# Kernel tuning notes

Measured on AMD Instinct MI355X. Metric: run time of the kernel, lower is better.

Reference implementation:

```python
import jax, jax.numpy as jnp
import numpy as np

B = 16        # batch
N = 1024      # satellite nodes
D = 256       # hidden size
H = 8         # attention heads
NUM_LAYERS = 3          # config.n_layer_aa
L = NUM_LAYERS + 1      # distinct GAT layers
EPS = 1e-5


def setup_inputs() -> dict:
    key = jax.random.key(0)
    ks = jax.random.split(key, 6)
    graph_vectors = jax.random.normal(ks[0], (B, N + 1, D), dtype=jnp.float32)
    graph = jax.random.uniform(ks[1], (B, N, N), dtype=jnp.float32)
    scale = 0.02
    Wq = jax.random.normal(ks[2], (L, D, D), dtype=jnp.float32) * scale
    Wk = jax.random.normal(ks[3], (L, D, D), dtype=jnp.float32) * scale
    Wv = jax.random.normal(ks[4], (L, D, D), dtype=jnp.float32) * scale
    Wo = jax.random.normal(ks[5], (L, D, D), dtype=jnp.float32) * scale
    ln_g = jnp.ones((L, D), dtype=jnp.float32)
    ln_b = jnp.zeros((L, D), dtype=jnp.float32)
    return {"graph_vectors": graph_vectors, "graph": graph,
            "Wq": Wq, "Wk": Wk, "Wv": Wv, "Wo": Wo,
            "ln_g": ln_g, "ln_b": ln_b}


def _layer_norm(x, g, b):
    mu = jnp.mean(x, axis=-1, keepdims=True)
    var = jnp.var(x, axis=-1, keepdims=True)
    return (x - mu) * jax.lax.rsqrt(var + EPS) * g + b


def _gat(x_q, x_kv, wq, wk, wv, wo, g, b):
    # multi-head attention: x_q [B,Lq,D] attends over x_kv [B,Lk,D]
    Bq, Lq, _ = x_q.shape
    Lk = x_kv.shape[1]
    dh = D // H
    q = (x_q @ wq).reshape(Bq, Lq, H, dh)
    k = (x_kv @ wk).reshape(Bq, Lk, H, dh)
    v = (x_kv @ wv).reshape(Bq, Lk, H, dh)
    scores = jnp.einsum('bqhd,bkhd->bhqk', q, k) / jnp.sqrt(jnp.float32(dh))
    attn = jax.nn.softmax(scores, axis=-1)
    o = jnp.einsum('bhqk,bkhd->bqhd', attn, v).reshape(Bq, Lq, D)
    out = o @ wo
    return _layer_norm(out + x_q, g, b)


def reference(graph_vectors, graph, Wq, Wk, Wv, Wo, ln_g, ln_b):
    relay = graph_vectors[:, :1, :]        # [B,1,D]
    sat = graph_vectors[:, 1:, :]          # [B,N,D]
    # layer 0: relay attends over satellites
    relay = _gat(relay, sat, Wq[0], Wk[0], Wv[0], Wo[0], ln_g[0], ln_b[0])
    # satellite = (satellite^T @ graph)^T -> [B,N,D]
    sat = jnp.einsum('bnd,bnm->bmd', sat, graph)
    gv = jnp.concatenate([relay, sat], axis=1)   # [B,N+1,D]
    # middle layers: full self-attention over all N+1 nodes
    for i in range(1, NUM_LAYERS):
        gv = _gat(gv, gv, Wq[i], Wk[i], Wv[i], Wo[i], ln_g[i], ln_b[i])
    relay_u = gv[:, :1, :]
    sat_u = gv[:, 1:, :]
    z = _gat(relay_u, sat_u, Wq[-1], Wk[-1], Wv[-1], Wo[-1], ln_g[-1], ln_b[-1])[:, 0, :]
    return z, sat_u
```

## Files before the change

### kernel.cpp

```cpp
#include <hip/hip_runtime.h>
#include <hip/hip_bf16.h>
#include <math.h>

#define BD   256
#define NH   8
#define DH   32
#define NB   16
#define NN   1024
#define LQ   1025
#define EPSV 1e-5f
#define KP   1088

typedef unsigned short ushort_t;
typedef __attribute__((ext_vector_type(8))) short short8;
typedef __attribute__((ext_vector_type(4))) float f32x4;

static __device__ __forceinline__ ushort_t f2b(float x) {
  union { __hip_bfloat16 h; ushort_t u; } cv;
  cv.h = __float2bfloat16(x);
  return cv.u;
}
static __device__ __forceinline__ float b2f(ushort_t u) {
  union { float f; unsigned v; } c; c.v = ((unsigned)u) << 16; return c.f;
}
static __device__ __forceinline__ float fexp2(float x) {
#if defined(__has_builtin)
#if __has_builtin(__builtin_amdgcn_exp2f)
  return __builtin_amdgcn_exp2f(x);
#else
  return exp2f(x);
#endif
#else
  return exp2f(x);
#endif
}
static __device__ __forceinline__ float wave_sum(float x) {
  #pragma unroll
  for (int off = 1; off < 64; off <<= 1) x += __shfl_xor(x, off);
  return x;
}
static __device__ __forceinline__ float wave_max(float x) {
  #pragma unroll
  for (int off = 1; off < 64; off <<= 1) x = fmaxf(x, __shfl_xor(x, off));
  return x;
}

__global__ void k_copy_cast(const float* __restrict__ in, float* __restrict__ X,
                            ushort_t* __restrict__ Xh, long n) {
  long stride = (long)gridDim.x * 256;
  for (long i = (long)blockIdx.x * 256 + threadIdx.x; i < n; i += stride) {
    float v = in[i];
    Xh[i] = f2b(v);
    long row = i >> 8;
    if (row % LQ == 0) X[i] = v;
  }
}

__global__ __launch_bounds__(256) void k_wtrans(const float* __restrict__ Wq,
                                                const float* __restrict__ Wk,
                                                const float* __restrict__ Wv,
                                                const float* __restrict__ Wo,
                                                ushort_t* __restrict__ Wt) {
  const float C1 = 0.17677669529663687f * 1.4426950408889634f;
  int mat = blockIdx.y;
  int type = mat >> 2, layer = mat & 3;
  const float* src = (type == 0) ? Wq : (type == 1) ? Wk : (type == 2) ? Wv : Wo;
  src += (long)layer * BD * BD;
  float scv = (type == 0) ? C1 : 1.f;
  ushort_t* dst = Wt + (long)mat * BD * BD;
  __shared__ float t[32][33];
  int k0 = (blockIdx.x & 7) * 32, n0 = (blockIdx.x >> 3) * 32;
  int tid = threadIdx.x;
  for (int i = tid; i < 1024; i += 256) {
    int kk = i >> 5, nn = i & 31;
    t[kk][nn] = src[(long)(k0 + kk) * BD + n0 + nn];
  }
  __syncthreads();
  for (int i = tid; i < 1024; i += 256) {
    int nn = i >> 5, kk = i & 31;
    dst[(long)(n0 + nn) * BD + k0 + kk] = f2b(t[kk][nn] * scv);
  }
}

__global__ __launch_bounds__(256) void k_gtrans(const float* __restrict__ G,
                                                ushort_t* __restrict__ Ght) {
  __shared__ ushort_t t[64][65];
  int b = blockIdx.y;
  int m0 = (blockIdx.x & 15) * 64, n0 = (blockIdx.x >> 4) * 64;
  const float* Gb = G + (long)b * NN * NN;
  ushort_t* dst = Ght + (long)b * NN * NN;
  int tid = threadIdx.x;
  #pragma unroll
  for (int rr = 0; rr < 16; rr++) {
    int n = rr * 4 + (tid >> 6);
    int m = tid & 63;
    t[m][n] = f2b(Gb[(long)(n0 + n) * NN + m0 + m]);
  }
  __syncthreads();
  #pragma unroll
  for (int rr = 0; rr < 8; rr++) {
    int m = rr * 8 + (tid >> 5);
    int n2 = (tid & 31) * 2;
    unsigned w = (unsigned)t[m][n2] | ((unsigned)t[m][n2 + 1] << 16);
    *(unsigned*)&dst[(long)(m0 + m) * NN + n0 + n2] = w;
  }
}

__global__ __launch_bounds__(256) void k_satT(const ushort_t* __restrict__ Xh,
                                              ushort_t* __restrict__ satT) {
  __shared__ ushort_t t[64][65];
  int b = blockIdx.y;
  int n0 = (blockIdx.x & 15) * 64, d0 = (blockIdx.x >> 4) * 64;
  const ushort_t* src = Xh + ((long)b * LQ + 1) * BD;
  ushort_t* dst = satT + (long)b * BD * NN;
  int tid = threadIdx.x;
  #pragma unroll
  for (int rr = 0; rr < 16; rr++) {
    int n = rr * 4 + (tid >> 6);
    int d = tid & 63;
    t[n][d] = src[(long)(n0 + n) * BD + d0 + d];
  }
  __syncthreads();
  #pragma unroll
  for (int rr = 0; rr < 8; rr++) {
    int d = rr * 8 + (tid >> 5);
    int n2 = (tid & 31) * 2;
    unsigned w = (unsigned)t[n2][d] | ((unsigned)t[n2 + 1][d] << 16);
    *(unsigned*)&dst[(long)(d0 + d) * NN + n0 + n2] = w;
  }
}

__global__ __launch_bounds__(256) void k_vtrans(const ushort_t* __restrict__ Vh,
                                                ushort_t* __restrict__ VhT) {
  __shared__ ushort_t t[64][65];
  int b = blockIdx.z;
  int n0 = blockIdx.x * 64, d0 = blockIdx.y * 64;
  const ushort_t* src = Vh + (long)b * LQ * BD;
  ushort_t* dst = VhT + (long)b * BD * KP;
  int tid = threadIdx.x;
  #pragma unroll
  for (int rr = 0; rr < 16; rr++) {
    int n = rr * 4 + (tid >> 6);
    int d = tid & 63;
    int key = n0 + n;
    t[n][d] = (key < LQ) ? src[(long)key * BD + d0 + d] : (ushort_t)0;
  }
  __syncthreads();
  #pragma unroll
  for (int rr = 0; rr < 8; rr++) {
    int d = rr * 8 + (tid >> 5);
    int n2 = (tid & 31) * 2;
    unsigned w = (unsigned)t[n2][d] | ((unsigned)t[n2 + 1][d] << 16);
    *(unsigned*)&dst[(long)(d0 + d) * KP + n0 + n2] = w;
  }
}

static __device__ __forceinline__ void core128(const ushort_t* __restrict__ A,
                                               const ushort_t* __restrict__ W,
                                               ushort_t* As, ushort_t* Bs,
                                               int M, int m0, int n0,
                                               float* __restrict__ Cf,
                                               ushort_t* __restrict__ Ch) {
  int tid = threadIdx.x;
  int wave = tid >> 6, lane = tid & 63;
  int l15 = lane & 15, quad = lane >> 4;
  int wr = wave >> 1, wc = wave & 1;

  int sr = tid >> 2, sc = (tid & 3) * 8;
  int ar0 = m0 + sr;      if (ar0 > M - 1) ar0 = M - 1;
  int ar1 = m0 + sr + 64; if (ar1 > M - 1) ar1 = M - 1;
  const ushort_t* aSrc0 = A + (long)ar0 * 256 + sc;
  const ushort_t* aSrc1 = A + (long)ar1 * 256 + sc;
  const ushort_t* bSrc0 = W + (long)(n0 + sr) * 256 + sc;
  const ushort_t* bSrc1 = bSrc0 + 64 * 256;
  ushort_t* aDst0 = &As[sr * 72 + sc];
  ushort_t* aDst1 = aDst0 + 64 * 72;
  ushort_t* bDst0 = &Bs[sr * 72 + sc];
  ushort_t* bDst1 = bDst0 + 64 * 72;

  {
    uint4 a0 = *(const uint4*)aSrc0;
    uint4 a1 = *(const uint4*)aSrc1;
    uint4 b0 = *(const uint4*)bSrc0;
    uint4 b1 = *(const uint4*)bSrc1;
    *(uint4*)aDst0 = a0; *(uint4*)aDst1 = a1;
    *(uint4*)bDst0 = b0; *(uint4*)bDst1 = b1;
  }
  __syncthreads();

  f32x4 acc[4][4];
  #pragma unroll
  for (int i = 0; i < 4; i++)
    #pragma unroll
    for (int j = 0; j < 4; j++) { acc[i][j][0] = 0.f; acc[i][j][1] = 0.f; acc[i][j][2] = 0.f; acc[i][j][3] = 0.f; }

  for (int ks = 0; ks < 8; ks++) {
    bool more = (ks < 7);
    uint4 na0, na1, nb0, nb1;
    if (more) {
      aSrc0 += 32; aSrc1 += 32; bSrc0 += 32; bSrc1 += 32;
      na0 = *(const uint4*)aSrc0;
      na1 = *(const uint4*)aSrc1;
      nb0 = *(const uint4*)bSrc0;
      nb1 = *(const uint4*)bSrc1;
    }
    short8 af[4], bf[4];
    #pragma unroll
    for (int f = 0; f < 4; f++)
      af[f] = *(const short8*)&As[(wr * 64 + f * 16 + l15) * 72 + quad * 8];
    #pragma unroll
    for (int f = 0; f < 4; f++)
      bf[f] = *(const short8*)&Bs[(wc * 64 + f * 16 + l15) * 72 + quad * 8];
    #pragma unroll
    for (int i = 0; i < 4; i++)
      #pragma unroll
      for (int j = 0; j < 4; j++)
        acc[i][j] = __builtin_amdgcn_mfma_f32_16x16x32_bf16(af[i], bf[j], acc[i][j], 0, 0, 0);
    if (more) {
      __syncthreads();
      *(uint4*)aDst0 = na0;
      *(uint4*)aDst1 = na1;
      *(uint4*)bDst0 = nb0;
      *(uint4*)bDst1 = nb1;
      __syncthreads();
    }
  }

  #pragma unroll
  for (int i = 0; i < 4; i++)
    #pragma unroll
    for (int j = 0; j < 4; j++)
      #pragma unroll
      for (int r = 0; r < 4; r++) {
        int m = m0 + wr * 64 + i * 16 + quad * 4 + r;
        if (m < M) {
          long idx = (long)m * 256 + n0 + wc * 64 + j * 16 + l15;
          if (Cf) Cf[idx] = acc[i][j][r];
          else    Ch[idx] = f2b(acc[i][j][r]);
        }
      }
}

__global__ __launch_bounds__(256) void gemm_qkv(const ushort_t* __restrict__ Xh,
                                                const ushort_t* __restrict__ Wt, int layer,
                                                ushort_t* __restrict__ Qo,
                                                ushort_t* __restrict__ Ko,
                                                ushort_t* __restrict__ Vo, int M) {
  __shared__ __align__(16) ushort_t As[128 * 72];
  __shared__ __align__(16) ushort_t Bs[128 * 72];
  int which = blockIdx.y >> 1;
  int n0 = (blockIdx.y & 1) * 128;
  const ushort_t* W = Wt + (long)(which * 4 + layer) * 65536;
  ushort_t* C = (which == 0) ? Qo : (which == 1) ? Ko : Vo;
  core128(Xh, W, As, Bs, M, blockIdx.x * 128, n0, nullptr, C);
}

__global__ __launch_bounds__(256) void gemm_kv(const ushort_t* __restrict__ Xh,
                                               const ushort_t* __restrict__ Wt, int layer,
                                               ushort_t* __restrict__ Ko,
                                               ushort_t* __restrict__ Vo) {
  __shared__ __align__(16) ushort_t As[128 * 72];
  __shared__ __align__(16) ushort_t Bs[128 * 72];
  int which = blockIdx.y >> 1;
  int n0 = (blockIdx.y & 1) * 128;
  int b = blockIdx.z;
  const ushort_t* W = Wt + (long)((which + 1) * 4 + layer) * 65536;
  const ushort_t* A = Xh + (long)b * (LQ * BD) + BD;
  ushort_t* C = ((which == 0) ? Ko : Vo) + (long)b * (NN * BD);
  core128(A, W, As, Bs, NN, blockIdx.x * 128, n0, nullptr, C);
}

__global__ __launch_bounds__(256) void gemm_oproj(const ushort_t* __restrict__ Oh,
                                                  const ushort_t* __restrict__ Wt, int layer,
                                                  float* __restrict__ Cf, int M) {
  __shared__ __align__(16) ushort_t As[128 * 72];
  __shared__ __align__(16) ushort_t Bs[128 * 72];
  core128(Oh, Wt + (long)(12 + layer) * 65536, As, Bs, M,
          blockIdx.x * 128, blockIdx.y * 128, Cf, nullptr);
}

__global__ __launch_bounds__(256) void gemm_gtx2(const ushort_t* __restrict__ Ght,
                                                 const ushort_t* __restrict__ satT,
                                                 float* __restrict__ X,
                                                 ushort_t* __restrict__ Xh) {
  __shared__ __align__(16) ushort_t As[128 * 72];
  __shared__ __align__(16) ushort_t Bs[128 * 72];
  int b = blockIdx.z;
  const ushort_t* A  = Ght + (long)b * NN * NN;
  const ushort_t* Bp = satT + (long)b * BD * NN;
  int tid = threadIdx.x;
  int wave = tid >> 6, lane = tid & 63;
  int l15 = lane & 15, quad = lane >> 4;
  int wr = wave >> 1, wc = wave & 1;
  int m0 = blockIdx.x * 128, d0 = blockIdx.y * 128;

  int sr = tid >> 2, sc = (tid & 3) * 8;
  const ushort_t* aSrc0 = A  + (long)(m0 + sr) * NN + sc;
  const ushort_t* aSrc1 = aSrc0 + (long)64 * NN;
  const ushort_t* bSrc0 = Bp + (long)(d0 + sr) * NN + sc;
  const ushort_t* bSrc1 = bSrc0 + (long)64 * NN;
  ushort_t* aDst0 = &As[sr * 72 + sc];
  ushort_t* aDst1 = aDst0 + 64 * 72;
  ushort_t* bDst0 = &Bs[sr * 72 + sc];
  ushort_t* bDst1 = bDst0 + 64 * 72;

  {
    uint4 a0 = *(const uint4*)aSrc0;
    uint4 a1 = *(const uint4*)aSrc1;
    uint4 b0 = *(const uint4*)bSrc0;
    uint4 b1 = *(const uint4*)bSrc1;
    *(uint4*)aDst0 = a0; *(uint4*)aDst1 = a1;
    *(uint4*)bDst0 = b0; *(uint4*)bDst1 = b1;
  }
  __syncthreads();

  f32x4 acc[4][4];
  #pragma unroll
  for (int i = 0; i < 4; i++)
    #pragma unroll
    for (int j = 0; j < 4; j++) { acc[i][j][0] = 0.f; acc[i][j][1] = 0.f; acc[i][j][2] = 0.f; acc[i][j][3] = 0.f; }

  for (int ks = 0; ks < 32; ks++) {
    bool more = (ks < 31);
    uint4 na0, na1, nb0, nb1;
    if (more) {
      aSrc0 += 32; aSrc1 += 32; bSrc0 += 32; bSrc1 += 32;
      na0 = *(const uint4*)aSrc0;
      na1 = *(const uint4*)aSrc1;
      nb0 = *(const uint4*)bSrc0;
      nb1 = *(const uint4*)bSrc1;
    }
    short8 af[4], bf[4];
    #pragma unroll
    for (int f = 0; f < 4; f++)
      af[f] = *(const short8*)&As[(wr * 64 + f * 16 + l15) * 72 + quad * 8];
    #pragma unroll
    for (int f = 0; f < 4; f++)
      bf[f] = *(const short8*)&Bs[(wc * 64 + f * 16 + l15) * 72 + quad * 8];
    #pragma unroll
    for (int i = 0; i < 4; i++)
      #pragma unroll
      for (int j = 0; j < 4; j++)
        acc[i][j] = __builtin_amdgcn_mfma_f32_16x16x32_bf16(af[i], bf[j], acc[i][j], 0, 0, 0);
    if (more) {
      __syncthreads();
      *(uint4*)aDst0 = na0;
      *(uint4*)aDst1 = na1;
      *(uint4*)bDst0 = nb0;
      *(uint4*)bDst1 = nb1;
      __syncthreads();
    }
  }

  long xb = ((long)b * LQ + 1) * 256;
  #pragma unroll
  for (int i = 0; i < 4; i++)
    #pragma unroll
    for (int j = 0; j < 4; j++)
      #pragma unroll
      for (int r = 0; r < 4; r++) {
        int m = m0 + wr * 64 + i * 16 + quad * 4 + r;
        int d = d0 + wc * 64 + j * 16 + l15;
        long idx = xb + (long)m * 256 + d;
        X[idx] = acc[i][j][r];
        Xh[idx] = f2b(acc[i][j][r]);
      }
}

__global__ __launch_bounds__(256) void attn_fa(const ushort_t* __restrict__ Qh,
                                               const ushort_t* __restrict__ Kh,
                                               const ushort_t* __restrict__ VhT,
                                               ushort_t* __restrict__ Oh) {
  __shared__ __align__(16) ushort_t Ps[4][32][72];
  __shared__ __align__(16) ushort_t Kb[64 * 72];
  __shared__ __align__(16) ushort_t Vb[32 * 72];
  __shared__ float Lbuf[4][32];
  int tid = threadIdx.x;
  int wave = tid >> 6, lane = tid & 63;
  int l15 = lane & 15, quad = lane >> 4;
  int b = blockIdx.x >> 3, h = blockIdx.x & 7;
  long hb = ((long)b * LQ) * BD + h * DH;
  long vB = (long)b * BD * KP;
  int hd0 = h * DH;
  int q0 = blockIdx.y * 128 + wave * 32;
  int lq = lane & 48;

  short8 qB[2];
  #pragma unroll
  for (int t = 0; t < 2; t++) {
    int qc = q0 + t * 16 + l15; if (qc > LQ - 1) qc = LQ - 1;
    qB[t] = *(const short8*)&Qh[hb + (long)qc * BD + quad * 8];
  }

  const ushort_t *s0, *s1;
  ushort_t *d0, *d1;
  long stp;
  if (wave < 2) {
    int kt0 = wave * 2, kt1 = kt0 + 1;
    s0 = Kh + hb + (long)(kt0 * 16 + l15) * BD + quad * 8;
    s1 = Kh + hb + (long)(kt1 * 16 + l15) * BD + quad * 8;
    d0 = &Kb[(kt0 * 16 + l15) * 72 + quad * 8];
    d1 = &Kb[(kt1 * 16 + l15) * 72 + quad * 8];
    stp = (long)64 * BD;
  } else {
    int sa = (wave - 2) * 2, sb = sa + 1;
    s0 = VhT + vB + (long)(hd0 + (sa >> 1) * 16 + l15) * KP + (sa & 1) * 32 + quad * 8;
    s1 = VhT + vB + (long)(hd0 + (sb >> 1) * 16 + l15) * KP + (sb & 1) * 32 + quad * 8;
    d0 = &Vb[((sa >> 1) * 16 + l15) * 72 + (sa & 1) * 32 + quad * 8];
    d1 = &Vb[((sb >> 1) * 16 + l15) * 72 + (sb & 1) * 32 + quad * 8];
    stp = 64;
  }
  {
    uint4 r0 = *(const uint4*)s0;
    uint4 r1 = *(const uint4*)s1;
    *(uint4*)d0 = r0;
    *(uint4*)d1 = r1;
  }
  __syncthreads();

  f32x4 o[2][2];
  #pragma unroll
  for (int t = 0; t < 2; t++)
    #pragma unroll
    for (int dt = 0; dt < 2; dt++) { o[t][dt][0] = 0.f; o[t][dt][1] = 0.f; o[t][dt][2] = 0.f; o[t][dt][3] = 0.f; }
  float m[2] = {-1e30f, -1e30f};
  float ls[2] = {0.f, 0.f};
  f32x4 zf; zf[0] = 0.f; zf[1] = 0.f; zf[2] = 0.f; zf[3] = 0.f;

  for (int c = 0; c < 17; c++) {
    bool more = (c < 16);
    uint4 n0, n1;
    if (more) {
      if (c == 15 && wave < 2) {
        const ushort_t* cl = Kh + hb + (long)(LQ - 1) * BD + quad * 8;
        n0 = *(const uint4*)cl;
        n1 = n0;
      } else {
        s0 += stp; s1 += stp;
        n0 = *(const uint4*)s0;
        n1 = *(const uint4*)s1;
      }
    }
    short8 ka[4];
    #pragma unroll
    for (int kt = 0; kt < 4; kt++)
      ka[kt] = *(const short8*)&Kb[(kt * 16 + l15) * 72 + quad * 8];

    bool tail = (c == 16);
    #pragma unroll
    for (int t = 0; t < 2; t++) {
      f32x4 s[4];
      #pragma unroll
      for (int kt = 0; kt < 4; kt++)
        s[kt] = __builtin_amdgcn_mfma_f32_16x16x32_bf16(ka[kt], qB[t], zf, 0, 0, 0);
      if (tail) {
        #pragma unroll
        for (int kt = 0; kt < 4; kt++)
          #pragma unroll
          for (int r = 0; r < 4; r++)
            if (kt + r) s[kt][r] = -1e30f;
        if (quad) s[0][0] = -1e30f;
      }
      float cm = fmaxf(fmaxf(s[0][0], s[0][1]), fmaxf(s[0][2], s[0][3]));
      cm = fmaxf(cm, fmaxf(fmaxf(s[1][0], s[1][1]), fmaxf(s[1][2], s[1][3])));
      cm = fmaxf(cm, fmaxf(fmaxf(s[2][0], s[2][1]), fmaxf(s[2][2], s[2][3])));
      cm = fmaxf(cm, fmaxf(fmaxf(s[3][0], s[3][1]), fmaxf(s[3][2], s[3][3])));
      cm = fmaxf(cm, __shfl_xor(cm, 16));
      cm = fmaxf(cm, __shfl_xor(cm, 32));
      if (__any(cm > m[t] + 8.f)) {
        float mn = fmaxf(m[t], cm);
        float f = fexp2(m[t] - mn);
        ls[t] *= f;
        m[t] = mn;
        #pragma unroll
        for (int r = 0; r < 4; r++) {
          float fr = __shfl(f, lq | (quad * 4 + r));
          o[t][0][r] *= fr;
          o[t][1][r] *= fr;
        }
      }
      float mt = m[t];
      #pragma unroll
      for (int kt = 0; kt < 4; kt++) {
        float p0 = fexp2(s[kt][0] - mt);
        float p1 = fexp2(s[kt][1] - mt);
        float p2 = fexp2(s[kt][2] - mt);
        float p3 = fexp2(s[kt][3] - mt);
        ls[t] += (p0 + p1) + (p2 + p3);
        unsigned lo = (unsigned)f2b(p0) | ((unsigned)f2b(p1) << 16);
        unsigned hi = (unsigned)f2b(p2) | ((unsigned)f2b(p3) << 16);
        uint2 w; w.x = lo; w.y = hi;
        *(uint2*)&Ps[wave][t * 16 + l15][kt * 16 + quad * 4] = w;
      }
    }
    short8 vb[2][2];
    #pragma unroll
    for (int dt = 0; dt < 2; dt++)
      #pragma unroll
      for (int ks = 0; ks < 2; ks++)
        vb[ks][dt] = *(const short8*)&Vb[(dt * 16 + l15) * 72 + ks * 32 + quad * 8];
    #pragma unroll
    for (int ks = 0; ks < 2; ks++) {
      short8 pa0 = *(const short8*)&Ps[wave][l15][ks * 32 + quad * 8];
      short8 pa1 = *(const short8*)&Ps[wave][16 + l15][ks * 32 + quad * 8];
      #pragma unroll
      for (int dt = 0; dt < 2; dt++) {
        o[0][dt] = __builtin_amdgcn_mfma_f32_16x16x32_bf16(pa0, vb[ks][dt], o[0][dt], 0, 0, 0);
        o[1][dt] = __builtin_amdgcn_mfma_f32_16x16x32_bf16(pa1, vb[ks][dt], o[1][dt], 0, 0, 0);
      }
    }
    if (more) {
      __syncthreads();
      *(uint4*)d0 = n0;
      *(uint4*)d1 = n1;
      __syncthreads();
    }
  }
  #pragma unroll
  for (int t = 0; t < 2; t++) {
    ls[t] += __shfl_xor(ls[t], 16);
    ls[t] += __shfl_xor(ls[t], 32);
  }
  if (quad == 0) {
    Lbuf[wave][l15] = ls[0];
    Lbuf[wave][16 + l15] = ls[1];
  }
  __syncthreads();
  #pragma unroll
  for (int mt = 0; mt < 2; mt++) {
    f32x4 lv = *(const f32x4*)&Lbuf[wave][mt * 16 + quad * 4];
    #pragma unroll
    for (int r = 0; r < 4; r++) {
      int row = q0 + mt * 16 + quad * 4 + r;
      if (row < LQ) {
        float den = lv[r];
        float inv = (den > 0.f) ? 1.f / den : 0.f;
        #pragma unroll
        for (int dt = 0; dt < 2; dt++)
          Oh[hb + (long)row * BD + dt * 16 + l15] = f2b(o[mt][dt][r] * inv);
      }
    }
  }
}

__global__ __launch_bounds__(256) void attn_relay(const float* __restrict__ X, long xstride,
                                                  const float* __restrict__ Wq,
                                                  const ushort_t* __restrict__ K,
                                                  const ushort_t* __restrict__ V,
                                                  float* __restrict__ o) {
  int b = blockIdx.x, h = blockIdx.y;
  int tid = threadIdx.x;
  int wave = tid >> 6, lane = tid & 63;
  const float scale = 0.17677669529663687f;
  __shared__ float s[NN];
  __shared__ float xs[BD];
  __shared__ float qs[DH];
  __shared__ float pmax[4], psum[4];
  __shared__ float part[8][33];
  xs[tid] = X[(long)b * xstride + tid];
  __syncthreads();
  {
    int d = tid & 31, slice = tid >> 5;
    const float* wq = Wq + h * DH + d;
    float partial = 0.f;
    #pragma unroll
    for (int kk = 0; kk < 32; kk++) {
      int k = slice * 32 + kk;
      partial += xs[k] * wq[(long)k * BD];
    }
    part[slice][d] = partial;
  }
  __syncthreads();
  if (tid < DH) {
    float ss = 0.f;
    #pragma unroll
    for (int t = 0; t < 8; t++) ss += part[t][tid];
    qs[tid] = ss;
  }
  __syncthreads();
  long base = ((long)b * NN) * BD + h * DH;
  float lm = -1e30f;
  for (int k = tid; k < NN; k += 256) {
    float dot = 0.f;
    const ushort_t* kr = &K[base + (long)k * BD];
    #pragma unroll
    for (int d2 = 0; d2 < 16; d2++) {
      unsigned w = *(const unsigned*)&kr[d2 * 2];
      dot += qs[d2 * 2] * b2f((ushort_t)(w & 0xffff)) + qs[d2 * 2 + 1] * b2f((ushort_t)(w >> 16));
    }
    float sv = dot * scale;
    s[k] = sv;
    lm = fmaxf(lm, sv);
  }
  lm = wave_max(lm);
  if (lane == 0) pmax[wave] = lm;
  __syncthreads();
  float mx = fmaxf(fmaxf(pmax[0], pmax[1]), fmaxf(pmax[2], pmax[3]));
  float sm = 0.f;
  for (int k = tid; k < NN; k += 256) {
    float p = __expf(s[k] - mx);
    s[k] = p;
    sm += p;
  }
  sm = wave_sum(sm);
  if (lane == 0) psum[wave] = sm;
  __syncthreads();
  float inv = 1.f / (((psum[0] + psum[1]) + (psum[2] + psum[3])));
  int d = tid & 31, slice = tid >> 5;
  float acc = 0.f;
  for (int k = slice; k < NN; k += 8) acc += s[k] * b2f(V[base + (long)k * BD + d]);
  part[slice][d] = acc;
  __syncthreads();
  if (tid < DH) {
    float ss = 0.f;
    #pragma unroll
    for (int t = 0; t < 8; t++) ss += part[t][tid];
    o[(long)b * BD + h * DH + tid] = ss * inv;
  }
}

__global__ __launch_bounds__(256) void rowvec_oproj_ln(const float* __restrict__ o,
                                                       const float* __restrict__ Wo,
                                                       const float* __restrict__ Xres, long xstride,
                                                       const float* __restrict__ g,
                                                       const float* __restrict__ beta,
                                                       float* __restrict__ dst, long dstride,
                                                       ushort_t* __restrict__ dsth, long dhstride) {
  int b = blockIdx.x, tid = threadIdx.x;
  int wave = tid >> 6, lane = tid & 63;
  __shared__ float xs[BD];
  __shared__ float ps[4], pq[4];
  xs[tid] = o[(long)b * BD + tid];
  __syncthreads();
  float acc = 0.f;
  for (int k = 0; k < BD; k++) acc += xs[k] * Wo[(long)k * BD + tid];
  float v = acc + Xres[(long)b * xstride + tid];
  float sum = wave_sum(v);
  float sq  = wave_sum(v * v);
  if (lane == 0) { ps[wave] = sum; pq[wave] = sq; }
  __syncthreads();
  float ts = (ps[0] + ps[1]) + (ps[2] + ps[3]);
  float tq = (pq[0] + pq[1]) + (pq[2] + pq[3]);
  float mu = ts * (1.f / BD);
  float var = tq * (1.f / BD) - mu * mu;
  float y = (v - mu) * rsqrtf(var + EPSV) * g[tid] + beta[tid];
  dst[(long)b * dstride + tid] = y;
  if (dsth) dsth[(long)b * dhstride + tid] = f2b(y);
}

__global__ __launch_bounds__(256) void ln_residual(const float* __restrict__ OP,
                                                   float* __restrict__ X,
                                                   ushort_t* __restrict__ Xh,
                                                   const float* __restrict__ g,
                                                   const float* __restrict__ beta,
                                                   float* __restrict__ sat_out) {
  long r = blockIdx.x;
  int tid = threadIdx.x;
  int wave = tid >> 6, lane = tid & 63;
  __shared__ float ps[4], pq[4];
  float v = OP[r * BD + tid] + X[r * BD + tid];
  float sum = wave_sum(v);
  float sq  = wave_sum(v * v);
  if (lane == 0) { ps[wave] = sum; pq[wave] = sq; }
  __syncthreads();
  float ts = (ps[0] + ps[1]) + (ps[2] + ps[3]);
  float tq = (pq[0] + pq[1]) + (pq[2] + pq[3]);
  float mu = ts * (1.f / BD);
  float var = tq * (1.f / BD) - mu * mu;
  float y = (v - mu) * rsqrtf(var + EPSV) * g[tid] + beta[tid];
  Xh[r * BD + tid] = f2b(y);
  if (sat_out) {
    long b = r / LQ;
    long rr = r - b * LQ;
    if (rr > 0)
      sat_out[(b * (long)NN + (rr - 1)) * BD + tid] = y;
    else
      X[r * BD + tid] = y;
  } else {
    X[r * BD + tid] = y;
  }
}

extern "C" void kernel_launch(void* const* d_in, const int* in_sizes, int n_in,
                              void* d_out, int out_size, void* d_ws, size_t ws_size,
                              hipStream_t stream) {
  const float* gv    = (const float*)d_in[0];
  const float* graph = (const float*)d_in[1];
  const float* Wq    = (const float*)d_in[2];
  const float* Wk    = (const float*)d_in[3];
  const float* Wv    = (const float*)d_in[4];
  const float* Wo    = (const float*)d_in[5];
  const float* lg    = (const float*)d_in[6];
  const float* lb    = (const float*)d_in[7];
  float* out = (float*)d_out;

  const long S  = (long)NB * LQ * BD;
  const long S4 = S * 4, S2 = S * 2;
  char* base = (char*)d_ws;
  float*    X    = (float*)base;
  ushort_t* Xh   = (ushort_t*)(base + S4);
  float*    B1   = (float*)(base + S4 + S2);
  ushort_t* Qh   = (ushort_t*)(base + 2 * S4 + S2);
  ushort_t* Kh   = (ushort_t*)(base + 2 * S4 + 2 * S2);
  ushort_t* Vh   = (ushort_t*)(base + 2 * S4 + 3 * S2);
  ushort_t* Oh   = (ushort_t*)(base + 2 * S4 + 4 * S2);
  ushort_t* Wt   = (ushort_t*)(base + 2 * S4 + 5 * S2);
  float*    orel = (float*)(base + 2 * S4 + 5 * S2 + 16L * 65536 * 2);
  ushort_t* Ght  = (ushort_t*)B1;
  ushort_t* satT = Vh;
  ushort_t* VhT  = (ushort_t*)B1;

  const long WSZ = (long)BD * BD;
  const long XST = (long)LQ * BD;
  dim3 blk(256);

  k_copy_cast<<<dim3(2048), blk, 0, stream>>>(gv, X, Xh, S);
  k_wtrans<<<dim3(64, 16), blk, 0, stream>>>(Wq, Wk, Wv, Wo, Wt);

  gemm_kv<<<dim3(8, 4, NB), blk, 0, stream>>>(Xh, Wt, 0, Kh, Vh);
  attn_relay<<<dim3(NB, NH), blk, 0, stream>>>(X, XST, Wq + 0 * WSZ, Kh, Vh, orel);
  rowvec_oproj_ln<<<dim3(NB), blk, 0, stream>>>(orel, Wo + 0 * WSZ, X, XST,
                                                lg + 0 * BD, lb + 0 * BD, X, XST, Xh, XST);

  k_gtrans<<<dim3(256, NB), blk, 0, stream>>>(graph, Ght);
  k_satT<<<dim3(64, NB), blk, 0, stream>>>(Xh, satT);
  gemm_gtx2<<<dim3(8, 2, NB), blk, 0, stream>>>(Ght, satT, X, Xh);

  for (int l = 1; l <= 2; l++) {
    gemm_qkv<<<dim3(129, 6), blk, 0, stream>>>(Xh, Wt, l, Qh, Kh, Vh, NB * LQ);
    k_vtrans<<<dim3(17, 4, NB), blk, 0, stream>>>(Vh, VhT);
    attn_fa<<<dim3(NB * NH, 9), blk, 0, stream>>>(Qh, Kh, VhT, Oh);
    gemm_oproj<<<dim3(129, 2), blk, 0, stream>>>(Oh, Wt, l, B1, NB * LQ);
    ln_residual<<<dim3(NB * LQ), blk, 0, stream>>>(B1, X, Xh, lg + l * BD, lb + l * BD,
                                                   (l == 2) ? (out + (long)NB * BD) : nullptr);
  }

  gemm_kv<<<dim3(8, 4, NB), blk, 0, stream>>>(Xh, Wt, 3, Kh, Vh);
  attn_relay<<<dim3(NB, NH), blk, 0, stream>>>(X, XST, Wq + 3 * WSZ, Kh, Vh, orel);
  rowvec_oproj_ln<<<dim3(NB), blk, 0, stream>>>(orel, Wo + 3 * WSZ, X, XST,
                                                lg + 3 * BD, lb + 3 * BD, out, BD, nullptr, 0);
}
```

Before: 502.3 us.

## Fuse V transpose into V projection GEMM epilogue and drop relay copy

The V projection is split out of the QKV GEMM into a new kernel that stages its output tile in shared memory and writes it directly in the transposed, padded layout that flash attention consumes. This removes the separate V-transpose kernel and its round trip of V through global memory. A small kernel zeroes the pad columns. The initial cast no longer copies relay rows into X; the relay attention reads the original input directly. The transposed store is strided per key row and may coalesce less well than the old transpose kernel.

```diff
diff --git a/kernel.cpp b/kernel.cpp
--- a/kernel.cpp
+++ b/kernel.cpp
@@ -45,15 +45,11 @@
   return x;
 }
 
-__global__ void k_copy_cast(const float* __restrict__ in, float* __restrict__ X,
+__global__ void k_copy_cast(const float* __restrict__ in,
                             ushort_t* __restrict__ Xh, long n) {
   long stride = (long)gridDim.x * 256;
-  for (long i = (long)blockIdx.x * 256 + threadIdx.x; i < n; i += stride) {
-    float v = in[i];
-    Xh[i] = f2b(v);
-    long row = i >> 8;
-    if (row % LQ == 0) X[i] = v;
-  }
+  for (long i = (long)blockIdx.x * 256 + threadIdx.x; i < n; i += stride)
+    Xh[i] = f2b(in[i]);
 }
 
 __global__ __launch_bounds__(256) void k_wtrans(const float* __restrict__ Wq,
@@ -130,29 +126,11 @@
   }
 }
 
-__global__ __launch_bounds__(256) void k_vtrans(const ushort_t* __restrict__ Vh,
-                                                ushort_t* __restrict__ VhT) {
-  __shared__ ushort_t t[64][65];
-  int b = blockIdx.z;
-  int n0 = blockIdx.x * 64, d0 = blockIdx.y * 64;
-  const ushort_t* src = Vh + (long)b * LQ * BD;
-  ushort_t* dst = VhT + (long)b * BD * KP;
-  int tid = threadIdx.x;
-  #pragma unroll
-  for (int rr = 0; rr < 16; rr++) {
-    int n = rr * 4 + (tid >> 6);
-    int d = tid & 63;
-    int key = n0 + n;
-    t[n][d] = (key < LQ) ? src[(long)key * BD + d0 + d] : (ushort_t)0;
-  }
-  __syncthreads();
-  #pragma unroll
-  for (int rr = 0; rr < 8; rr++) {
-    int d = rr * 8 + (tid >> 5);
-    int n2 = (tid & 31) * 2;
-    unsigned w = (unsigned)t[n2][d] | ((unsigned)t[n2 + 1][d] << 16);
-    *(unsigned*)&dst[(long)(d0 + d) * KP + n0 + n2] = w;
-  }
+__global__ __launch_bounds__(256) void k_vpad(ushort_t* __restrict__ VhT) {
+  int b = blockIdx.x, d = threadIdx.x;
+  ushort_t* row = VhT + (long)b * BD * KP + (long)d * KP + LQ;
+  #pragma unroll
+  for (int k = 0; k < KP - LQ; k++) row[k] = 0;
 }
 
 static __device__ __forceinline__ void core128(const ushort_t* __restrict__ A,
@@ -244,15 +222,114 @@
 __global__ __launch_bounds__(256) void gemm_qkv(const ushort_t* __restrict__ Xh,
                                                 const ushort_t* __restrict__ Wt, int layer,
                                                 ushort_t* __restrict__ Qo,
-                                                ushort_t* __restrict__ Ko,
-                                                ushort_t* __restrict__ Vo, int M) {
+                                                ushort_t* __restrict__ Ko, int M) {
   __shared__ __align__(16) ushort_t As[128 * 72];
   __shared__ __align__(16) ushort_t Bs[128 * 72];
   int which = blockIdx.y >> 1;
   int n0 = (blockIdx.y & 1) * 128;
   const ushort_t* W = Wt + (long)(which * 4 + layer) * 65536;
-  ushort_t* C = (which == 0) ? Qo : (which == 1) ? Ko : Vo;
+  ushort_t* C = (which == 0) ? Qo : Ko;
   core128(Xh, W, As, Bs, M, blockIdx.x * 128, n0, nullptr, C);
+}
+
+__global__ __launch_bounds__(256) void gemm_vT(const ushort_t* __restrict__ Xh,
+                                               const ushort_t* __restrict__ Wt, int layer,
+                                               ushort_t* __restrict__ VhT, int M) {
+  __shared__ __align__(16) char smem[36864];
+  ushort_t* As = (ushort_t*)smem;
+  ushort_t* Bs = As + 128 * 72;
+  ushort_t* Ls = (ushort_t*)smem;
+  const ushort_t* W = Wt + (long)(8 + layer) * 65536;
+  int tid = threadIdx.x;
+  int wave = tid >> 6, lane = tid & 63;
+  int l15 = lane & 15, quad = lane >> 4;
+  int wr = wave >> 1, wc = wave & 1;
+  int m0 = blockIdx.x * 128, n0 = blockIdx.y * 128;
+
+  int sr = tid >> 2, sc = (tid & 3) * 8;
+  int ar0 = m0 + sr;      if (ar0 > M - 1) ar0 = M - 1;
+  int ar1 = m0 + sr + 64; if (ar1 > M - 1) ar1 = M - 1;
+  const ushort_t* aSrc0 = Xh + (long)ar0 * 256 + sc;
+  const ushort_t* aSrc1 = Xh + (long)ar1 * 256 + sc;
+  const ushort_t* bSrc0 = W + (long)(n0 + sr) * 256 + sc;
+  const ushort_t* bSrc1 = bSrc0 + 64 * 256;
+  ushort_t* aDst0 = &As[sr * 72 + sc];
+  ushort_t* aDst1 = aDst0 + 64 * 72;
+  ushort_t* bDst0 = &Bs[sr * 72 + sc];
+  ushort_t* bDst1 = bDst0 + 64 * 72;
+
+  {
+    uint4 a0 = *(const uint4*)aSrc0;
+    uint4 a1 = *(const uint4*)aSrc1;
+    uint4 b0 = *(const uint4*)bSrc0;
+    uint4 b1 = *(const uint4*)bSrc1;
+    *(uint4*)aDst0 = a0; *(uint4*)aDst1 = a1;
+    *(uint4*)bDst0 = b0; *(uint4*)bDst1 = b1;
+  }
+  __syncthreads();
+
+  f32x4 acc[4][4];
+  #pragma unroll
+  for (int i = 0; i < 4; i++)
+    #pragma unroll
+    for (int j = 0; j < 4; j++) { acc[i][j][0] = 0.f; acc[i][j][1] = 0.f; acc[i][j][2] = 0.f; acc[i][j][3] = 0.f; }
+
+  for (int ks = 0; ks < 8; ks++) {
+    bool more = (ks < 7);
+    uint4 na0, na1, nb0, nb1;
+    if (more) {
+      aSrc0 += 32; aSrc1 += 32; bSrc0 += 32; bSrc1 += 32;
+      na0 = *(const uint4*)aSrc0;
+      na1 = *(const uint4*)aSrc1;
+      nb0 = *(const uint4*)bSrc0;
+      nb1 = *(const uint4*)bSrc1;
+    }
+    short8 af[4], bf[4];
+    #pragma unroll
+    for (int f = 0; f < 4; f++)
+      af[f] = *(const short8*)&As[(wr * 64 + f * 16 + l15) * 72 + quad * 8];
+    #pragma unroll
+    for (int f = 0; f < 4; f++)
+      bf[f] = *(const short8*)&Bs[(wc * 64 + f * 16 + l15) * 72 + quad * 8];
+    #pragma unroll
+    for (int i = 0; i < 4; i++)
+      #pragma unroll
+      for (int j = 0; j < 4; j++)
+        acc[i][j] = __builtin_amdgcn_mfma_f32_16x16x32_bf16(af[i], bf[j], acc[i][j], 0, 0, 0);
+    if (more) {
+      __syncthreads();
+      *(uint4*)aDst0 = na0;
+      *(uint4*)aDst1 = na1;
+      *(uint4*)bDst0 = nb0;
+      *(uint4*)bDst1 = nb1;
+      __syncthreads();
+    }
+  }
+
+  __syncthreads();
+  #pragma unroll
+  for (int i = 0; i < 4; i++)
+    #pragma unroll
+    for (int j = 0; j < 4; j++)
+      #pragma unroll
+      for (int r = 0; r < 4; r++) {
+        int ml = wr * 64 + i * 16 + quad * 4 + r;
+        int nl = wc * 64 + j * 16 + l15;
+        Ls[ml * 130 + nl] = f2b(acc[i][j][r]);
+      }
+  __syncthreads();
+  int b_lo = m0 / LQ;
+  int m_sw = (b_lo + 1) * LQ;
+  for (int rr = 0; rr < 64; rr++) {
+    int idx = rr * 256 + tid;
+    int n = idx >> 7, kk = idx & 127;
+    int mg = m0 + kk;
+    if (mg < M) {
+      int bb = (mg >= m_sw) ? (b_lo + 1) : b_lo;
+      int key = mg - bb * LQ;
+      VhT[(long)bb * BD * KP + (long)(n0 + n) * KP + key] = Ls[kk * 130 + n];
+    }
+  }
 }
 
 __global__ __launch_bounds__(256) void gemm_kv(const ushort_t* __restrict__ Xh,
@@ -714,12 +791,12 @@
   const long XST = (long)LQ * BD;
   dim3 blk(256);
 
-  k_copy_cast<<<dim3(2048), blk, 0, stream>>>(gv, X, Xh, S);
+  k_copy_cast<<<dim3(2048), blk, 0, stream>>>(gv, Xh, S);
   k_wtrans<<<dim3(64, 16), blk, 0, stream>>>(Wq, Wk, Wv, Wo, Wt);
 
   gemm_kv<<<dim3(8, 4, NB), blk, 0, stream>>>(Xh, Wt, 0, Kh, Vh);
-  attn_relay<<<dim3(NB, NH), blk, 0, stream>>>(X, XST, Wq + 0 * WSZ, Kh, Vh, orel);
-  rowvec_oproj_ln<<<dim3(NB), blk, 0, stream>>>(orel, Wo + 0 * WSZ, X, XST,
+  attn_relay<<<dim3(NB, NH), blk, 0, stream>>>(gv, XST, Wq + 0 * WSZ, Kh, Vh, orel);
+  rowvec_oproj_ln<<<dim3(NB), blk, 0, stream>>>(orel, Wo + 0 * WSZ, gv, XST,
                                                 lg + 0 * BD, lb + 0 * BD, X, XST, Xh, XST);
 
   k_gtrans<<<dim3(256, NB), blk, 0, stream>>>(graph, Ght);
@@ -727,8 +804,9 @@
   gemm_gtx2<<<dim3(8, 2, NB), blk, 0, stream>>>(Ght, satT, X, Xh);
 
   for (int l = 1; l <= 2; l++) {
-    gemm_qkv<<<dim3(129, 6), blk, 0, stream>>>(Xh, Wt, l, Qh, Kh, Vh, NB * LQ);
-    k_vtrans<<<dim3(17, 4, NB), blk, 0, stream>>>(Vh, VhT);
+    gemm_qkv<<<dim3(129, 4), blk, 0, stream>>>(Xh, Wt, l, Qh, Kh, NB * LQ);
+    gemm_vT<<<dim3(129, 2), blk, 0, stream>>>(Xh, Wt, l, VhT, NB * LQ);
+    k_vpad<<<dim3(NB), blk, 0, stream>>>(VhT);
     attn_fa<<<dim3(NB * NH, 9), blk, 0, stream>>>(Qh, Kh, VhT, Oh);
     gemm_oproj<<<dim3(129, 2), blk, 0, stream>>>(Oh, Wt, l, B1, NB * LQ);
     ln_residual<<<dim3(NB * LQ), blk, 0, stream>>>(B1, X, Xh, lg + l * BD, lb + l * BD,
```

Measured after the change: 508.8 us. No clear change (+1.3%).
